# Optimization experiments

Measured on AMD Instinct MI355X. Metric: run time of the kernel, lower is better.

The kernel has to match this reference:

```python
import jax, jax.numpy as jnp
import numpy as np

N_HEADS = 16
D_EMBED = 1024
D_HEAD = D_EMBED // N_HEADS
CAUSAL = True


def setup_inputs() -> dict:
    key = jax.random.key(0)
    k1, k2, k3, k4, k5 = jax.random.split(key, 5)
    B, S = 2, 2048
    scale = 1.0 / np.sqrt(D_EMBED)
    return {
        "x": jax.random.normal(k1, (B, S, D_EMBED), dtype=jnp.float32),
        "Wqkv": jax.random.normal(k2, (D_EMBED, 3 * D_EMBED), dtype=jnp.float32) * scale,
        "bqkv": jax.random.normal(k3, (3 * D_EMBED,), dtype=jnp.float32) * 0.01,
        "Wo": jax.random.normal(k4, (D_EMBED, D_EMBED), dtype=jnp.float32) * scale,
        "bo": jax.random.normal(k5, (D_EMBED,), dtype=jnp.float32) * 0.01,
    }


def reference(x, Wqkv, bqkv, Wo, bo):
    B, S, D = x.shape
    qkv = x @ Wqkv + bqkv                      # [B,S,3D]
    q, k, v = jnp.split(qkv, 3, axis=-1)
    # [B,S,D] -> [B,H,S,dh]
    def heads(t):
        return t.reshape(B, S, N_HEADS, D_HEAD).transpose(0, 2, 1, 3)
    q, k, v = heads(q), heads(k), heads(v)
    scores = jnp.einsum('bhqd,bhkd->bhqk', q, k)
    if CAUSAL:
        mask = jnp.triu(jnp.ones((S, S), dtype=bool), k=1)  # True above diagonal
        scores = jnp.where(mask, -jnp.inf, scores)
    scores = scores / jnp.sqrt(jnp.asarray(D_HEAD, dtype=scores.dtype))
    attn = jax.nn.softmax(scores, axis=-1)
    out = jnp.einsum('bhqk,bhkd->bhqd', attn, v)           # [B,H,S,dh]
    out = out.transpose(0, 2, 1, 3).reshape(B, S, D)
    return out @ Wo + bo
```

## Files before the change

kernel.cpp:

```cpp
#include <hip/hip_runtime.h>
#include <hip/hip_bf16.h>
#include <cstdint>
#include <cstddef>


using bf16 = __hip_bfloat16;
typedef __attribute__((ext_vector_type(8))) short short8;
typedef __attribute__((ext_vector_type(4))) float f32x4;
typedef __attribute__((ext_vector_type(16))) float f32x16;
typedef __attribute__((ext_vector_type(4))) unsigned int u32x4;

__device__ __forceinline__ unsigned short f2b(float f) {
    bf16 h = __float2bfloat16(f);
    return *reinterpret_cast<unsigned short*>(&h);
}

__device__ __forceinline__ void async16(const void* g, void* l) {
    __builtin_amdgcn_global_load_lds(
        (const __attribute__((address_space(1))) void*)g,
        (__attribute__((address_space(3))) void*)l, 16, 0, 0);
}

__global__ __launch_bounds__(256) void cvt_kernel(const float* __restrict__ in,
                                                  bf16* __restrict__ out, int n4) {
    int i = blockIdx.x * 256 + threadIdx.x;
    if (i >= n4) return;
    const float4 v = reinterpret_cast<const float4*>(in)[i];
    ushort4 o;
    o.x = f2b(v.x); o.y = f2b(v.y); o.z = f2b(v.z); o.w = f2b(v.w);
    reinterpret_cast<ushort4*>(out)[i] = o;
}

__global__ __launch_bounds__(256) void transpose_cvt(const float* __restrict__ in,
                                                     bf16* __restrict__ out,
                                                     int K, int N) {
    __shared__ float tile[32][33];
    int n0 = blockIdx.x * 32, k0 = blockIdx.y * 32;
    int tx = threadIdx.x, ty = threadIdx.y;
    #pragma unroll
    for (int i = 0; i < 32; i += 8)
        tile[ty + i][tx] = in[(size_t)(k0 + ty + i) * N + n0 + tx];
    __syncthreads();
    #pragma unroll
    for (int i = 0; i < 32; i += 8)
        out[(size_t)(n0 + ty + i) * K + k0 + tx] = __float2bfloat16(tile[tx][ty + i]);
}

template <int EPI>
__global__ __launch_bounds__(256) void gemm_bt(
    const bf16* __restrict__ A,
    const bf16* __restrict__ Bt,
    const float* __restrict__ bias,
    float* __restrict__ Cf,
    bf16* __restrict__ qd, bf16* __restrict__ kd, bf16* __restrict__ vtd,
    int M, int N, int K) {
    __shared__ bf16 As[128 * 32];
    __shared__ bf16 Bs[128 * 32];
    const int t = threadIdx.x;
    const int lane = t & 63;
    const int lr = lane & 15, lg = lane >> 4;
    const int wave = t >> 6;
    const int wr = wave >> 1, wc = wave & 1;
    const int m0 = blockIdx.x * 128, n0 = blockIdx.y * 128;

    const bf16* aSrc = A + (size_t)(m0 + (t >> 2)) * K + (t & 3) * 8;
    const bf16* bSrc = Bt + (size_t)(n0 + (t >> 2)) * K + (t & 3) * 8;
    bf16* aDst0 = &As[t * 8];
    bf16* aDst1 = &As[2048 + t * 8];
    bf16* bDst0 = &Bs[t * 8];
    bf16* bDst1 = &Bs[2048 + t * 8];
    const size_t rowStep = (size_t)64 * K;

    f32x4 acc[4][4] = {};

    for (int k0 = 0; k0 < K; k0 += 32) {
        __syncthreads();
        async16(aSrc + k0, aDst0);
        async16(aSrc + rowStep + k0, aDst1);
        async16(bSrc + k0, bDst0);
        async16(bSrc + rowStep + k0, bDst1);
        __syncthreads();
        short8 af[4], bfr[4];
        #pragma unroll
        for (int i = 0; i < 4; ++i)
            af[i] = *reinterpret_cast<const short8*>(
                &As[(wr * 64 + i * 16 + lr) * 32 + lg * 8]);
        #pragma unroll
        for (int i = 0; i < 4; ++i)
            bfr[i] = *reinterpret_cast<const short8*>(
                &Bs[(wc * 64 + i * 16 + lr) * 32 + lg * 8]);
        #pragma unroll
        for (int mi = 0; mi < 4; ++mi)
            #pragma unroll
            for (int ni = 0; ni < 4; ++ni)
                acc[mi][ni] = __builtin_amdgcn_mfma_f32_16x16x32_bf16(
                    af[mi], bfr[ni], acc[mi][ni], 0, 0, 0);
    }

    #pragma unroll
    for (int mi = 0; mi < 4; ++mi) {
        #pragma unroll
        for (int ni = 0; ni < 4; ++ni) {
            #pragma unroll
            for (int r = 0; r < 4; ++r) {
                const int row = m0 + wr * 64 + mi * 16 + lg * 4 + r;
                const int col = n0 + wc * 64 + ni * 16 + lr;
                const float v = acc[mi][ni][r] + bias[col];
                if constexpr (EPI == 0) {
                    Cf[(size_t)row * N + col] = v;
                } else {
                    const bf16 hv = __float2bfloat16(v);
                    const int part = col >> 10;
                    const int within = col & 1023;
                    const int h = within >> 6, d = within & 63;
                    const int b = row >> 11, s = row & 2047;
                    const int bh = b * 16 + h;
                    if (part == 0)
                        qd[((size_t)bh * 2048 + s) * 64 + d] = hv;
                    else if (part == 1)
                        kd[((size_t)bh * 2048 + s) * 64 + d] = hv;
                    else
                        vtd[((size_t)bh * 64 + d) * 2048 + s] = hv;
                }
            }
        }
    }
}

__global__ __launch_bounds__(256, 2) void attn_kernel(const bf16* __restrict__ q,
                                                      const bf16* __restrict__ k,
                                                      const bf16* __restrict__ vt,
                                                      bf16* __restrict__ o) {
    const int S = 2048;
    const int f = blockIdx.x;
    const int res = f & 7, m = f >> 3;
    const int grp = m >> 4;
    const int bh = res + 8 * grp;
    const int bxr = m & 15;
    const int bx = (grp & 2) ? (15 - bxr) : bxr;
    const int b = bh >> 4, h = bh & 15;
    const int w = threadIdx.x >> 6;
    const int u = w >> 1, par = w & 1;
    const int lane = threadIdx.x & 63;
    const int ln = lane & 31;
    const int hi = lane >> 5;
    const int P = 2 * (15 - bx) + u;
    const int qbaseA = P * 64;
    const int qbaseB = P * 64 + 32;

    const bf16* qp = q + (size_t)bh * S * 64;
    const bf16* kp = k + (size_t)bh * S * 64;
    const bf16* vp = vt + (size_t)bh * 64 * S;

    short8 qfA[4], qfB[4];
    #pragma unroll
    for (int i = 0; i < 4; ++i) {
        qfA[i] = *reinterpret_cast<const short8*>(
            &qp[(size_t)(qbaseA + ln) * 64 + i * 16 + hi * 8]);
        qfB[i] = *reinterpret_cast<const short8*>(
            &qp[(size_t)(qbaseB + ln) * 64 + i * 16 + hi * 8]);
    }

    f32x16 oA0 = {}, oA1 = {}, oB0 = {}, oB1 = {};
    f32x4 lsvA = {0.f, 0.f, 0.f, 0.f}, lsvB = {0.f, 0.f, 0.f, 0.f};

    short8 kA[4], kB[4], vA[4], vB[4];

    auto kload = [&](short8 (&kf)[4], int tile) {
        const bf16* base = &kp[(size_t)(tile * 32 + ln) * 64 + hi * 8];
        #pragma unroll
        for (int i = 0; i < 4; ++i)
            kf[i] = *reinterpret_cast<const short8*>(base + i * 16);
    };
    auto vload = [&](short8 (&vf)[4], int tile) {
        #pragma unroll
        for (int dblk = 0; dblk < 2; ++dblk)
            #pragma unroll
            for (int half = 0; half < 2; ++half)
                vf[dblk * 2 + half] = *reinterpret_cast<const short8*>(
                    &vp[(size_t)(dblk * 32 + ln) * S + tile * 32 + half * 16 +
                        hi * 8]);
    };

    auto body = [&](const short8 (&kf)[4], const short8 (&vf)[4],
                    const short8 (&qf)[4], f32x16& o0, f32x16& o1, f32x4& lsv,
                    bool diag) {
        f32x16 z0 = {}, z1 = {};
        z0 = __builtin_amdgcn_mfma_f32_32x32x16_bf16(kf[0], qf[0], z0, 0, 0, 0);
        z0 = __builtin_amdgcn_mfma_f32_32x32x16_bf16(kf[1], qf[1], z0, 0, 0, 0);
        z1 = __builtin_amdgcn_mfma_f32_32x32x16_bf16(kf[2], qf[2], z1, 0, 0, 0);
        z1 = __builtin_amdgcn_mfma_f32_32x32x16_bf16(kf[3], qf[3], z1, 0, 0, 0);
        const f32x16 z = z0 + z1;
        f32x16 pv;
        #pragma unroll
        for (int r = 0; r < 16; ++r) {
            const int kreg = (r & 3) + 8 * (r >> 2) + 4 * hi;
            float e = __expf(z[r] * 0.125f);
            if (diag && (kreg > ln)) e = 0.f;
            pv[r] = e;
            lsv[r & 3] += e;
        }
        unsigned a0, a1, b0, b1, c0, c1, d0, d1;
        asm("v_cvt_pk_bf16_f32 %0, %1, %2" : "=v"(a0) : "v"(pv[0]), "v"(pv[1]));
        asm("v_cvt_pk_bf16_f32 %0, %1, %2" : "=v"(a1) : "v"(pv[2]), "v"(pv[3]));
        asm("v_cvt_pk_bf16_f32 %0, %1, %2" : "=v"(b0) : "v"(pv[4]), "v"(pv[5]));
        asm("v_cvt_pk_bf16_f32 %0, %1, %2" : "=v"(b1) : "v"(pv[6]), "v"(pv[7]));
        asm("v_cvt_pk_bf16_f32 %0, %1, %2" : "=v"(c0) : "v"(pv[8]), "v"(pv[9]));
        asm("v_cvt_pk_bf16_f32 %0, %1, %2" : "=v"(c1) : "v"(pv[10]), "v"(pv[11]));
        asm("v_cvt_pk_bf16_f32 %0, %1, %2" : "=v"(d0) : "v"(pv[12]), "v"(pv[13]));
        asm("v_cvt_pk_bf16_f32 %0, %1, %2" : "=v"(d1) : "v"(pv[14]), "v"(pv[15]));
        asm("v_permlane32_swap_b32 %0, %1" : "+v"(a0), "+v"(b0));
        asm("v_permlane32_swap_b32 %0, %1" : "+v"(a1), "+v"(b1));
        asm("v_permlane32_swap_b32 %0, %1" : "+v"(c0), "+v"(d0));
        asm("v_permlane32_swap_b32 %0, %1" : "+v"(c1), "+v"(d1));
        u32x4 t0, t1;
        t0[0] = a0; t0[1] = a1; t0[2] = b0; t0[3] = b1;
        t1[0] = c0; t1[1] = c1; t1[2] = d0; t1[3] = d1;
        const short8 pa0 = __builtin_bit_cast(short8, t0);
        const short8 pa1 = __builtin_bit_cast(short8, t1);
        o0 = __builtin_amdgcn_mfma_f32_32x32x16_bf16(pa0, vf[0], o0, 0, 0, 0);
        o0 = __builtin_amdgcn_mfma_f32_32x32x16_bf16(pa1, vf[1], o0, 0, 0, 0);
        o1 = __builtin_amdgcn_mfma_f32_32x32x16_bf16(pa0, vf[2], o1, 0, 0, 0);
        o1 = __builtin_amdgcn_mfma_f32_32x32x16_bf16(pa1, vf[3], o1, 0, 0, 0);
    };

    auto dual = [&](const short8 (&kf)[4], const short8 (&vf)[4]) {
        body(kf, vf, qfA, oA0, oA1, lsvA, false);
        body(kf, vf, qfB, oB0, oB1, lsvB, false);
    };
    auto final_body = [&](const short8 (&kf)[4], const short8 (&vf)[4]) {
        if (par == 0) {
            body(kf, vf, qfA, oA0, oA1, lsvA, true);
            body(kf, vf, qfB, oB0, oB1, lsvB, false);
        } else {
            body(kf, vf, qfB, oB0, oB1, lsvB, true);
        }
    };

    kload(kA, par);
    vload(vA, par);
    int i = 0;
    for (; i + 2 <= P; i += 2) {
        kload(kB, par + 2 * (i + 1));
        vload(vB, par + 2 * (i + 1));
        dual(kA, vA);
        kload(kA, par + 2 * (i + 2));
        vload(vA, par + 2 * (i + 2));
        dual(kB, vB);
    }
    if (i < P) {
        kload(kB, par + 2 * P);
        vload(vB, par + 2 * P);
        dual(kA, vA);
        final_body(kB, vB);
    } else {
        final_body(kA, vA);
    }

    float lsA = (lsvA[0] + lsvA[1]) + (lsvA[2] + lsvA[3]);
    float lsB = (lsvB[0] + lsvB[1]) + (lsvB[2] + lsvB[3]);

    __shared__ float red[2][64][65];
    __shared__ float redl[2][64][2];
    if (par == 1) {
        float* dst = red[u][lane];
        #pragma unroll
        for (int r = 0; r < 16; ++r) {
            dst[r] = oA0[r];
            dst[16 + r] = oA1[r];
            dst[32 + r] = oB0[r];
            dst[48 + r] = oB1[r];
        }
        redl[u][lane][0] = lsA;
        redl[u][lane][1] = lsB;
    }
    __syncthreads();
    if (par == 1) return;
    {
        const float* src = red[u][lane];
        #pragma unroll
        for (int r = 0; r < 16; ++r) {
            oA0[r] += src[r];
            oA1[r] += src[16 + r];
            oB0[r] += src[32 + r];
            oB1[r] += src[48 + r];
        }
        lsA += redl[u][lane][0];
        lsB += redl[u][lane][1];
    }

    lsA += __shfl_xor(lsA, 32, 64);
    lsB += __shfl_xor(lsB, 32, 64);
    const float myInvA = 1.0f / lsA;
    const float myInvB = 1.0f / lsB;
    #pragma unroll
    for (int r = 0; r < 16; ++r) {
        const int qrow = (r & 3) + 8 * (r >> 2) + 4 * hi;
        const float invA = __shfl(myInvA, qrow, 64);
        const float invB = __shfl(myInvB, qrow, 64);
        const size_t rowA = ((size_t)b * S + qbaseA + qrow) * 1024 + h * 64;
        const size_t rowB = ((size_t)b * S + qbaseB + qrow) * 1024 + h * 64;
        o[rowA + ln] = __float2bfloat16(oA0[r] * invA);
        o[rowA + 32 + ln] = __float2bfloat16(oA1[r] * invA);
        o[rowB + ln] = __float2bfloat16(oB0[r] * invB);
        o[rowB + 32 + ln] = __float2bfloat16(oB1[r] * invB);
    }
}

extern "C" void kernel_launch(void* const* d_in, const int* in_sizes, int n_in,
                              void* d_out, int out_size, void* d_ws, size_t ws_size,
                              hipStream_t stream) {
    const float* x = (const float*)d_in[0];
    const float* Wqkv = (const float*)d_in[1];
    const float* bqkv = (const float*)d_in[2];
    const float* Wo = (const float*)d_in[3];
    const float* bo = (const float*)d_in[4];
    float* out = (float*)d_out;
    char* ws = (char*)d_ws;

    bf16* x_bf = (bf16*)(ws);
    bf16* wqkv_t = (bf16*)(ws + 8388608);
    bf16* wo_t = (bf16*)(ws + 14680064);
    bf16* qb = (bf16*)(ws + 16777216);
    bf16* kb = (bf16*)(ws + 25165824);
    bf16* vtb = (bf16*)(ws + 33554432);
    bf16* attn_o = x_bf;

    cvt_kernel<<<4096, 256, 0, stream>>>(x, x_bf, 1048576);
    transpose_cvt<<<dim3(96, 32), dim3(32, 8), 0, stream>>>(Wqkv, wqkv_t, 1024, 3072);
    transpose_cvt<<<dim3(32, 32), dim3(32, 8), 0, stream>>>(Wo, wo_t, 1024, 1024);
    gemm_bt<1><<<dim3(32, 24), 256, 0, stream>>>(x_bf, wqkv_t, bqkv, nullptr, qb, kb,
                                                 vtb, 4096, 3072, 1024);
    attn_kernel<<<512, 256, 0, stream>>>(qb, kb, vtb, attn_o);
    gemm_bt<0><<<dim3(32, 8), 256, 0, stream>>>(attn_o, wo_t, bo, out, nullptr,
                                                nullptr, nullptr, 4096, 1024, 1024);
}
```

Before: 129.0 us.

## Replace QKV GEMM with 256x256-tile 8-phase pipelined kernel using swizzled LDS

Adds a dedicated QKV projection kernel with 256x256 tiles and 512 threads. It double-buffers K-chunks in LDS through async global-to-LDS loads, applies an XOR swizzle to avoid bank conflicts, and interleaves loads with MFMA phases using barriers and s_setprio. Workgroup ids are remapped for L2 locality. The goal is to hide memory latency and reuse more data per block than the old 128x128 kernel. The cost is a larger LDS footprint and only 192 blocks, so the grid may not fill all CUs evenly.

```diff
diff --git a/kernel.cpp b/kernel.cpp
--- a/kernel.cpp
+++ b/kernel.cpp
@@ -46,13 +46,157 @@
         out[(size_t)(n0 + ty + i) * K + k0 + tx] = __float2bfloat16(tile[tx][ty + i]);
 }
 
+#define BAR __builtin_amdgcn_s_barrier()
+#define LGKM0 asm volatile("s_waitcnt lgkmcnt(0)" ::: "memory")
+#define VM4 asm volatile("s_waitcnt vmcnt(4)" ::: "memory")
+#define VM0 asm volatile("s_waitcnt vmcnt(0)" ::: "memory")
+#define PRIO1 __builtin_amdgcn_s_setprio(1)
+#define PRIO0 __builtin_amdgcn_s_setprio(0)
+
+#define PH_READ_A(D, KS, MO)                                              \
+    {                                                                     \
+        _Pragma("unroll") for (int mi = 0; mi < 4; ++mi)                  \
+            af[mi] = *reinterpret_cast<const short8*>(                    \
+                &As[D][KS][(arow0 + ((MO) + mi) * 16) * 32 + swz]);       \
+    }
+#define PH_READ_B(D, KS)                                                  \
+    {                                                                     \
+        _Pragma("unroll") for (int ni = 0; ni < 4; ++ni)                  \
+            bfv[ni] = *reinterpret_cast<const short8*>(                   \
+                &Bs[D][KS][(brow0 + ni * 16) * 32 + swz]);                \
+    }
+#define MFMA16(MO)                                                        \
+    {                                                                     \
+        _Pragma("unroll") for (int mi = 0; mi < 4; ++mi) {                \
+            _Pragma("unroll") for (int ni = 0; ni < 4; ++ni) {            \
+                acc[(MO) + mi][ni] = __builtin_amdgcn_mfma_f32_16x16x32_bf16( \
+                    af[mi], bfv[ni], acc[(MO) + mi][ni], 0, 0, 0);        \
+            }                                                             \
+        }                                                                 \
+    }
+
+__global__ __launch_bounds__(512, 2) void gemm_qkv_8ph(
+    const bf16* __restrict__ A,
+    const bf16* __restrict__ Bt,
+    const float* __restrict__ bias,
+    bf16* __restrict__ qd, bf16* __restrict__ kd, bf16* __restrict__ vtd) {
+    constexpr int Kd = 1024;
+    constexpr int NT = Kd / 64;
+    __shared__ bf16 As[2][2][256 * 32];
+    __shared__ bf16 Bs[2][2][256 * 32];
+
+    const int tid = threadIdx.x;
+    const int wave = tid >> 6, lane = tid & 63;
+    const int lr = lane & 15, lg = lane >> 4;
+    const int wr = wave >> 2, wc = wave & 3;
+
+    const int orig = blockIdx.x;
+    const int wg = (orig & 7) * 24 + (orig >> 3);
+    const int bx = wg / 12, by = wg % 12;
+    const int m0 = bx * 256, n0 = by * 256;
+
+    int s_row[2], s_col[2];
+    #pragma unroll
+    for (int j = 0; j < 2; ++j) {
+        const int p = j * 8192 + tid * 16;
+        const int row = p >> 6;
+        const int c = ((p >> 4) & 3) ^ (row & 3);
+        s_row[j] = row;
+        s_col[j] = c * 8;
+    }
+
+    auto stageA = [&](int d, int ks, int kt) {
+        const int kb = kt * 64 + ks * 32;
+        #pragma unroll
+        for (int j = 0; j < 2; ++j)
+            async16(A + (size_t)(m0 + s_row[j]) * Kd + kb + s_col[j],
+                    &As[d][ks][j * 4096 + tid * 8]);
+    };
+    auto stageB = [&](int d, int ks, int kt) {
+        const int kb = kt * 64 + ks * 32;
+        #pragma unroll
+        for (int j = 0; j < 2; ++j)
+            async16(Bt + (size_t)(n0 + s_row[j]) * Kd + kb + s_col[j],
+                    &Bs[d][ks][j * 4096 + tid * 8]);
+    };
+
+    const int swz = (lg ^ (lr & 3)) * 8;
+    const int arow0 = wr * 128 + lr;
+    const int brow0 = wc * 64 + lr;
+
+    f32x4 acc[8][4] = {};
+    short8 af[4], bfv[4];
+
+    stageA(0, 0, 0);
+    stageB(0, 0, 0);
+    stageA(0, 1, 0);
+    stageB(0, 1, 0);
+    VM4;
+    BAR;
+
+    for (int kt = 0; kt < NT - 1; ++kt) {
+        const int d = kt & 1;
+        const int kn = kt + 1;
+        PH_READ_B(d, 0);
+        PH_READ_A(d, 0, 0);
+        stageA(d ^ 1, 0, kn);
+        BAR; LGKM0; PRIO1; MFMA16(0); PRIO0; BAR;
+        PH_READ_A(d, 0, 4);
+        stageB(d ^ 1, 0, kn);
+        BAR; LGKM0; PRIO1; MFMA16(4); PRIO0; VM4; BAR;
+        PH_READ_B(d, 1);
+        PH_READ_A(d, 1, 0);
+        stageA(d ^ 1, 1, kn);
+        BAR; LGKM0; PRIO1; MFMA16(0); PRIO0; BAR;
+        PH_READ_A(d, 1, 4);
+        stageB(d ^ 1, 1, kn);
+        BAR; LGKM0; PRIO1; MFMA16(4); PRIO0; VM4; BAR;
+    }
+    {
+        PH_READ_B(1, 0);
+        PH_READ_A(1, 0, 0);
+        BAR; LGKM0; PRIO1; MFMA16(0); PRIO0; BAR;
+        PH_READ_A(1, 0, 4);
+        BAR; LGKM0; PRIO1; MFMA16(4); PRIO0; VM0; BAR;
+        PH_READ_B(1, 1);
+        PH_READ_A(1, 1, 0);
+        BAR; LGKM0; PRIO1; MFMA16(0); PRIO0; BAR;
+        PH_READ_A(1, 1, 4);
+        BAR; LGKM0; PRIO1; MFMA16(4); PRIO0;
+    }
+
+    #pragma unroll
+    for (int mi = 0; mi < 8; ++mi) {
+        #pragma unroll
+        for (int ni = 0; ni < 4; ++ni) {
+            #pragma unroll
+            for (int r = 0; r < 4; ++r) {
+                const int row = m0 + wr * 128 + mi * 16 + lg * 4 + r;
+                const int col = n0 + wc * 64 + ni * 16 + lr;
+                const float v = acc[mi][ni][r] + bias[col];
+                const bf16 hv = __float2bfloat16(v);
+                const int part = col >> 10;
+                const int within = col & 1023;
+                const int h = within >> 6, dd = within & 63;
+                const int b = row >> 11, s = row & 2047;
+                const int bh = b * 16 + h;
+                if (part == 0)
+                    qd[((size_t)bh * 2048 + s) * 64 + dd] = hv;
+                else if (part == 1)
+                    kd[((size_t)bh * 2048 + s) * 64 + dd] = hv;
+                else
+                    vtd[((size_t)bh * 64 + dd) * 2048 + s] = hv;
+            }
+        }
+    }
+}
+
 template <int EPI>
 __global__ __launch_bounds__(256) void gemm_bt(
     const bf16* __restrict__ A,
     const bf16* __restrict__ Bt,
     const float* __restrict__ bias,
     float* __restrict__ Cf,
-    bf16* __restrict__ qd, bf16* __restrict__ kd, bf16* __restrict__ vtd,
     int M, int N, int K) {
     __shared__ bf16 As[128 * 32];
     __shared__ bf16 Bs[128 * 32];
@@ -105,23 +249,7 @@
             for (int r = 0; r < 4; ++r) {
                 const int row = m0 + wr * 64 + mi * 16 + lg * 4 + r;
                 const int col = n0 + wc * 64 + ni * 16 + lr;
-                const float v = acc[mi][ni][r] + bias[col];
-                if constexpr (EPI == 0) {
-                    Cf[(size_t)row * N + col] = v;
-                } else {
-                    const bf16 hv = __float2bfloat16(v);
-                    const int part = col >> 10;
-                    const int within = col & 1023;
-                    const int h = within >> 6, d = within & 63;
-                    const int b = row >> 11, s = row & 2047;
-                    const int bh = b * 16 + h;
-                    if (part == 0)
-                        qd[((size_t)bh * 2048 + s) * 64 + d] = hv;
-                    else if (part == 1)
-                        kd[((size_t)bh * 2048 + s) * 64 + d] = hv;
-                    else
-                        vtd[((size_t)bh * 64 + d) * 2048 + s] = hv;
-                }
+                Cf[(size_t)row * N + col] = acc[mi][ni][r] + bias[col];
             }
         }
     }
@@ -329,9 +457,8 @@
     cvt_kernel<<<4096, 256, 0, stream>>>(x, x_bf, 1048576);
     transpose_cvt<<<dim3(96, 32), dim3(32, 8), 0, stream>>>(Wqkv, wqkv_t, 1024, 3072);
     transpose_cvt<<<dim3(32, 32), dim3(32, 8), 0, stream>>>(Wo, wo_t, 1024, 1024);
-    gemm_bt<1><<<dim3(32, 24), 256, 0, stream>>>(x_bf, wqkv_t, bqkv, nullptr, qb, kb,
-                                                 vtb, 4096, 3072, 1024);
+    gemm_qkv_8ph<<<192, 512, 0, stream>>>(x_bf, wqkv_t, bqkv, qb, kb, vtb);
     attn_kernel<<<512, 256, 0, stream>>>(qb, kb, vtb, attn_o);
-    gemm_bt<0><<<dim3(32, 8), 256, 0, stream>>>(attn_o, wo_t, bo, out, nullptr,
-                                                nullptr, nullptr, 4096, 1024, 1024);
-}
+    gemm_bt<0><<<dim3(32, 8), 256, 0, stream>>>(attn_o, wo_t, bo, out,
+                                                4096, 1024, 1024);
+}
```

Result: slower. 144.9 us (+12.4%).
